# Optimization experiments

Measured on AMD Instinct MI355X. Metric: run time of the kernel, lower is better.

## Reference

```python
import jax, jax.numpy as jnp
import numpy as np

N_CONTENT = 100000
N_USER = 100000
N_EDGES = 1600000
D_CONTENT = 256
D_USER = 128
HIDDEN = 128
OUT = 64


def setup_inputs() -> dict:
    key = jax.random.key(0)
    ks = jax.random.split(key, 12)
    s = lambda d: 1.0 / np.sqrt(d)
    return {
        "x_content": jax.random.normal(ks[0], (N_CONTENT, D_CONTENT), jnp.float32),
        "x_user": jax.random.normal(ks[1], (N_USER, D_USER), jnp.float32),
        # edge_index[0] = source (user) ids, edge_index[1] = destination (content) ids
        "edge_index": jax.random.randint(ks[2], (2, N_EDGES), 0, N_CONTENT, jnp.int64),
        # per-node-type input projections
        "Wc": jax.random.normal(ks[3], (D_CONTENT, HIDDEN), jnp.float32) * s(D_CONTENT),
        "bc": jnp.zeros((HIDDEN,), jnp.float32),
        "Wu": jax.random.normal(ks[4], (D_USER, HIDDEN), jnp.float32) * s(D_USER),
        "bu": jnp.zeros((HIDDEN,), jnp.float32),
        # SAGEConv: W_l applied to aggregated neighbor features (with bias),
        # W_r applied to root/self features (no bias, per PyG default)
        "Wl": jax.random.normal(ks[5], (HIDDEN, HIDDEN), jnp.float32) * s(HIDDEN),
        "bl": jnp.zeros((HIDDEN,), jnp.float32),
        "Wr": jax.random.normal(ks[6], (HIDDEN, HIDDEN), jnp.float32) * s(HIDDEN),
        # final output projection on content nodes
        "Wo": jax.random.normal(ks[7], (HIDDEN, OUT), jnp.float32) * s(HIDDEN),
        "bo": jnp.zeros((OUT,), jnp.float32),
    }


def reference(x_content, x_user, edge_index, Wc, bc, Wu, bu, Wl, bl, Wr, Wo, bo):
    # Per-node-type linear + relu
    h_c = jax.nn.relu(x_content @ Wc + bc)  # [Nc, H]
    h_u = jax.nn.relu(x_user @ Wu + bu)      # [Nu, H]

    src, dst = edge_index[0], edge_index[1]
    # SAGEConv mean aggregation: gather user features along edges, scatter-mean to content
    msg = h_u[src]                                              # [E, H] gather
    agg = jax.ops.segment_sum(msg, dst, num_segments=N_CONTENT) # [Nc, H]
    cnt = jax.ops.segment_sum(jnp.ones((msg.shape[0],), msg.dtype), dst,
                              num_segments=N_CONTENT)
    mean = agg / jnp.maximum(cnt, 1.0)[:, None]                 # 0 for isolated nodes

    h = mean @ Wl + bl + h_c @ Wr                               # SAGE combine
    return h @ Wo + bo                                          # [Nc, OUT]
```

## Files before the change

kernel.cpp:

```cpp
#include <hip/hip_runtime.h>
#include <hip/hip_bf16.h>

#define NC 100000
#define NU 100000
#define NE 1600000
#define DC 256
#define DU 128
#define HID 128
#define OUTD 64

#define BSHIFT 9
#define BRANGE 512
#define NBUCK ((NC + BRANGE - 1) / BRANGE)
#define BCAP 10240
#define EPB 8192
#define ABLK ((NE + EPB - 1) / EPB)

#define TM 32
#define NT_C (NC / TM)
#define NT_U (NU / TM)

#define SH (HID + 8)

typedef __attribute__((ext_vector_type(8))) short bf16x8;
typedef __attribute__((ext_vector_type(4))) float f32x4;

__device__ inline unsigned short f2b(float f) {
    unsigned int u = __float_as_uint(f);
    u += 0x7fffu + ((u >> 16) & 1u);
    return (unsigned short)(u >> 16);
}

__global__ void prep_kernel(const float* __restrict__ Wl, const float* __restrict__ bl,
                            const float* __restrict__ Wr, const float* __restrict__ Wo,
                            const float* __restrict__ bo,
                            __hip_bfloat16* __restrict__ Wlo_p,
                            __hip_bfloat16* __restrict__ Wro_p,
                            float* __restrict__ b2) {
    const int k = blockIdx.x;
    const int t = threadIdx.x;
    const int f = t & 63, j4 = t >> 6;
    __shared__ float red[3][4][OUTD];
    float a0 = 0.f, a1 = 0.f, s = 0.f;
    for (int m = j4 * 32; m < j4 * 32 + 32; ++m) {
        float wo = Wo[m * OUTD + f];
        a0 = fmaf(Wl[k * HID + m], wo, a0);
        a1 = fmaf(Wr[k * HID + m], wo, a1);
        s = fmaf(bl[m], wo, s);
    }
    red[0][j4][f] = a0; red[1][j4][f] = a1; red[2][j4][f] = s;
    __syncthreads();
    if (j4 == 0) {
        a0 = red[0][0][f] + red[0][1][f] + red[0][2][f] + red[0][3][f];
        a1 = red[1][0][f] + red[1][1][f] + red[1][2][f] + red[1][3][f];
        const int wv = f >> 4, l16 = f & 15;
        const int ks = k >> 5, quad = (k >> 3) & 3, e = k & 7;
        const int idx = (((wv * 4 + ks) * 64) + quad * 16 + l16) * 8 + e;
        Wlo_p[idx] = __float2bfloat16(a0);
        Wro_p[idx] = __float2bfloat16(a1);
        if (k == 0)
            b2[f] = bo[f] + red[2][0][f] + red[2][1][f] + red[2][2][f] + red[2][3][f];
    }
}

__global__ void pack_w(const float* __restrict__ W, __hip_bfloat16* __restrict__ Wp,
                       int K) {
    int i = blockIdx.x * blockDim.x + threadIdx.x;
    int total = K * HID;
    if (i >= total) return;
    int j = i % HID, k = i / HID;
    int nks = K >> 5;
    int idx = (((j >> 4) * nks + (k >> 5)) * 64 + ((k >> 3) & 3) * 16 + (j & 15)) * 8 +
              (k & 7);
    Wp[idx] = __float2bfloat16(W[k * HID + j]);
}

template <int DIN, bool BF16OUT>
__device__ __forceinline__ void gemm_path(const float* __restrict__ x,
                                          const __hip_bfloat16* __restrict__ W1p,
                                          const float* __restrict__ b1,
                                          const __hip_bfloat16* __restrict__ W2p,
                                          const float* __restrict__ bias2,
                                          void* __restrict__ outp, int tile,
                                          short* __restrict__ smem) {
    constexpr int NKS = DIN / 32;
    constexpr int SA = DIN + 8;
    constexpr int CPR = DIN / 8;
    constexpr int RSTEP = 256 / CPR;
    constexpr int NCH = TM / RSTEP;
    short* a_s = smem;
    short* h_s = smem + TM * SA;

    const int t = threadIdx.x;
    const int w = t >> 6, lane = t & 63;
    const int quad = lane >> 4, l16 = lane & 15;
    const int r0 = t / CPR, c0 = t % CPR;
    const int base = tile * TM;

    bf16x8 b1f[2][NKS];
#pragma unroll
    for (int ntl = 0; ntl < 2; ++ntl)
#pragma unroll
        for (int ks = 0; ks < NKS; ++ks)
            b1f[ntl][ks] =
                *(const bf16x8*)&W1p[(size_t)(((2 * w + ntl) * NKS + ks) * 64 + lane) * 8];
    bf16x8 b2f[HID / 32];
#pragma unroll
    for (int ks = 0; ks < HID / 32; ++ks)
        b2f[ks] = *(const bf16x8*)&W2p[(size_t)((w * 4 + ks) * 64 + lane) * 8];
    const float bb1_0 = b1[w * 32 + l16];
    const float bb1_1 = b1[w * 32 + 16 + l16];
    const float bb2 = BF16OUT ? 0.f : bias2[w * 16 + l16];

    float4 va[NCH][2];
#pragma unroll
    for (int k = 0; k < NCH; ++k) {
        const float4* p = (const float4*)(x + (size_t)(base + r0 + k * RSTEP) * DIN + c0 * 8);
        va[k][0] = p[0];
        va[k][1] = p[1];
    }
#pragma unroll
    for (int k = 0; k < NCH; ++k) {
        bf16x8 a;
        a[0] = (short)f2b(va[k][0].x); a[1] = (short)f2b(va[k][0].y);
        a[2] = (short)f2b(va[k][0].z); a[3] = (short)f2b(va[k][0].w);
        a[4] = (short)f2b(va[k][1].x); a[5] = (short)f2b(va[k][1].y);
        a[6] = (short)f2b(va[k][1].z); a[7] = (short)f2b(va[k][1].w);
        *(bf16x8*)&a_s[(r0 + k * RSTEP) * SA + c0 * 8] = a;
    }
    __syncthreads();

#pragma unroll
    for (int rg = 0; rg < TM / 16; ++rg) {
        bf16x8 af[NKS];
#pragma unroll
        for (int ks = 0; ks < NKS; ++ks)
            af[ks] = *(const bf16x8*)&a_s[(rg * 16 + l16) * SA + ks * 32 + quad * 8];
        f32x4 acc0 = (f32x4){0.f, 0.f, 0.f, 0.f};
        f32x4 acc1 = (f32x4){0.f, 0.f, 0.f, 0.f};
#pragma unroll
        for (int ks = 0; ks < NKS; ++ks) {
            acc0 = __builtin_amdgcn_mfma_f32_16x16x32_bf16(af[ks], b1f[0][ks], acc0, 0, 0, 0);
            acc1 = __builtin_amdgcn_mfma_f32_16x16x32_bf16(af[ks], b1f[1][ks], acc1, 0, 0, 0);
        }
#pragma unroll
        for (int r = 0; r < 4; ++r) {
            int row = rg * 16 + quad * 4 + r;
            h_s[row * SH + w * 32 + l16] = (short)f2b(fmaxf(acc0[r] + bb1_0, 0.f));
            h_s[row * SH + w * 32 + 16 + l16] = (short)f2b(fmaxf(acc1[r] + bb1_1, 0.f));
        }
    }
    __syncthreads();

#pragma unroll
    for (int rg = 0; rg < TM / 16; ++rg) {
        f32x4 acc = (f32x4){0.f, 0.f, 0.f, 0.f};
#pragma unroll
        for (int ks = 0; ks < HID / 32; ++ks) {
            bf16x8 a = *(const bf16x8*)&h_s[(rg * 16 + l16) * SH + ks * 32 + quad * 8];
            acc = __builtin_amdgcn_mfma_f32_16x16x32_bf16(a, b2f[ks], acc, 0, 0, 0);
        }
#pragma unroll
        for (int r = 0; r < 4; ++r) {
            int rr = base + rg * 16 + quad * 4 + r;
            if (BF16OUT)
                ((unsigned short*)outp)[(size_t)rr * OUTD + w * 16 + l16] = f2b(acc[r]);
            else
                ((float*)outp)[(size_t)rr * OUTD + w * 16 + l16] = acc[r] + bb2;
        }
    }
}

__global__ void __launch_bounds__(256, 4) dual_gemm(
    const float* __restrict__ xc, const __hip_bfloat16* __restrict__ Wc_p,
    const float* __restrict__ bc, const __hip_bfloat16* __restrict__ Wro_p,
    const float* __restrict__ b2, float* __restrict__ out,
    const float* __restrict__ xu, const __hip_bfloat16* __restrict__ Wu_p,
    const float* __restrict__ bu, const __hip_bfloat16* __restrict__ Wlo_p,
    unsigned short* __restrict__ pu) {
    __shared__ __align__(16) short smem[TM * (DC + 8) + TM * (HID + 8)];
    int b = blockIdx.x;
    if (b < NT_C)
        gemm_path<DC, false>(xc, Wc_p, bc, Wro_p, b2, out, b, smem);
    else
        gemm_path<DU, true>(xu, Wu_p, bu, Wlo_p, nullptr, pu, b - NT_C, smem);
}

__global__ void __launch_bounds__(256) bucket_a(const int* __restrict__ src,
                                                const int* __restrict__ dst,
                                                int* __restrict__ gcur,
                                                unsigned int* __restrict__ bke) {
    __shared__ unsigned int pk[EPB];
    __shared__ int hist[NBUCK];
    __shared__ int lbase[NBUCK];
    __shared__ int lcur[NBUCK];
    __shared__ int gb[NBUCK];
    __shared__ int ts[256];
    const int t = threadIdx.x;
    const int base = blockIdx.x * EPB;
    for (int i = t; i < NBUCK; i += 256) hist[i] = 0;
    __syncthreads();
#pragma unroll
    for (int k = 0; k < EPB / 256; ++k) {
        int e = base + k * 256 + t;
        if (e < NE) atomicAdd(&hist[dst[e] >> BSHIFT], 1);
    }
    __syncthreads();
    int h = (t < NBUCK) ? hist[t] : 0;
    ts[t] = h;
    __syncthreads();
    for (int d = 1; d < 256; d <<= 1) {
        int x = (t >= d) ? ts[t - d] : 0;
        __syncthreads();
        ts[t] += x;
        __syncthreads();
    }
    if (t < NBUCK) {
        int ex = ts[t] - h;
        lbase[t] = ex;
        lcur[t] = ex;
        gb[t] = atomicAdd(&gcur[t], h);
    }
    __syncthreads();
#pragma unroll
    for (int k = 0; k < EPB / 256; ++k) {
        int e = base + k * 256 + t;
        if (e < NE) {
            int s = src[e], d = dst[e];
            int b = d >> BSHIFT;
            int p = atomicAdd(&lcur[b], 1);
            pk[p] = ((unsigned int)s << BSHIFT) | (unsigned int)(d & (BRANGE - 1));
        }
    }
    __syncthreads();
    const int wv = t >> 6, ln = t & 63;
    for (int b = wv; b < NBUCK; b += 4) {
        int s0 = lbase[b], c = hist[b], g0 = gb[b];
        for (int j = ln; j < c; j += 64) {
            int pos = g0 + j;
            if (pos < BCAP) bke[(size_t)b * BCAP + pos] = pk[s0 + j];
        }
    }
}

__global__ void scan_mid(const int* __restrict__ gcur, int* __restrict__ gbase,
                         int* __restrict__ off) {
    __shared__ int ts[256];
    int t = threadIdx.x;
    int h = (t < NBUCK) ? gcur[t] : 0;
    ts[t] = h;
    __syncthreads();
    for (int d = 1; d < 256; d <<= 1) {
        int x = (t >= d) ? ts[t - d] : 0;
        __syncthreads();
        ts[t] += x;
        __syncthreads();
    }
    if (t < NBUCK) gbase[t] = ts[t] - h;
    if (t == 0) { gbase[NBUCK] = NE; off[NC] = NE; }
}

__global__ void __launch_bounds__(256) bucket_b(const int* __restrict__ gcur,
                                                const int* __restrict__ gbase,
                                                const unsigned int* __restrict__ bke,
                                                int* __restrict__ off,
                                                int* __restrict__ ssrc) {
    __shared__ unsigned int pk[BCAP];
    __shared__ int hist[BRANGE];
    __shared__ int hb[BRANGE];
    __shared__ int cur[BRANGE];
    __shared__ int ts[256];
    const int t = threadIdx.x;
    const int b = blockIdx.x;
    const int n = min(gcur[b], BCAP);
    const int g0 = gbase[b];
    for (int i = t; i < n; i += 256) pk[i] = bke[(size_t)b * BCAP + i];
    for (int i = t; i < BRANGE; i += 256) hist[i] = 0;
    __syncthreads();
    for (int i = t; i < n; i += 256) atomicAdd(&hist[pk[i] & (BRANGE - 1)], 1);
    __syncthreads();
    int a0 = hist[2 * t], a1 = hist[2 * t + 1];
    int s = a0 + a1;
    ts[t] = s;
    __syncthreads();
    for (int d = 1; d < 256; d <<= 1) {
        int x = (t >= d) ? ts[t - d] : 0;
        __syncthreads();
        ts[t] += x;
        __syncthreads();
    }
    int ex = ts[t] - s;
    hb[2 * t] = ex;
    hb[2 * t + 1] = ex + a0;
    __syncthreads();
    for (int i = t; i < BRANGE; i += 256) {
        int node = b * BRANGE + i;
        cur[i] = g0 + hb[i];
        if (node < NC) off[node] = g0 + hb[i];
    }
    __syncthreads();
    for (int i = t; i < n; i += 256) {
        unsigned int v = pk[i];
        int p = atomicAdd(&cur[v & (BRANGE - 1)], 1);
        ssrc[p] = (int)(v >> BSHIFT);
    }
}

__global__ void __launch_bounds__(256) gather_agg(const int* __restrict__ ssrc,
                                                  const int* __restrict__ off,
                                                  const unsigned int* __restrict__ pu,
                                                  float* __restrict__ out) {
    int node = blockIdx.x * 4 + (threadIdx.x >> 6);
    if (node >= NC) return;
    int lane = threadIdx.x & 63;
    int g = lane >> 3;
    int f8 = lane & 7;
    int e0 = off[node], e1 = off[node + 1];
    float acc[8] = {0.f, 0.f, 0.f, 0.f, 0.f, 0.f, 0.f, 0.f};
    for (int e = e0 + g; e < e1; e += 8) {
        int s = ssrc[e];
        uint4 v = ((const uint4*)pu)[(size_t)s * 8 + f8];
        acc[0] += __uint_as_float(v.x << 16);
        acc[1] += __uint_as_float(v.x & 0xffff0000u);
        acc[2] += __uint_as_float(v.y << 16);
        acc[3] += __uint_as_float(v.y & 0xffff0000u);
        acc[4] += __uint_as_float(v.z << 16);
        acc[5] += __uint_as_float(v.z & 0xffff0000u);
        acc[6] += __uint_as_float(v.w << 16);
        acc[7] += __uint_as_float(v.w & 0xffff0000u);
    }
#pragma unroll
    for (int m = 8; m <= 32; m <<= 1) {
#pragma unroll
        for (int j = 0; j < 8; ++j) acc[j] += __shfl_xor(acc[j], m, 64);
    }
    if (g == 0) {
        float inv = 1.0f / (float)max(e1 - e0, 1);
        float4* po = (float4*)(out + (size_t)node * OUTD + f8 * 8);
        float4 o0 = po[0], o1 = po[1];
        o0.x += acc[0] * inv; o0.y += acc[1] * inv;
        o0.z += acc[2] * inv; o0.w += acc[3] * inv;
        o1.x += acc[4] * inv; o1.y += acc[5] * inv;
        o1.z += acc[6] * inv; o1.w += acc[7] * inv;
        po[0] = o0; po[1] = o1;
    }
}

extern "C" void kernel_launch(void* const* d_in, const int* in_sizes, int n_in,
                              void* d_out, int out_size, void* d_ws, size_t ws_size,
                              hipStream_t stream) {
    const float* xc = (const float*)d_in[0];
    const float* xu = (const float*)d_in[1];
    const int*   ei = (const int*)d_in[2];
    const float* Wc = (const float*)d_in[3];
    const float* bc = (const float*)d_in[4];
    const float* Wu = (const float*)d_in[5];
    const float* bu = (const float*)d_in[6];
    const float* Wl = (const float*)d_in[7];
    const float* bl = (const float*)d_in[8];
    const float* Wr = (const float*)d_in[9];
    const float* Wo = (const float*)d_in[10];
    const float* bo = (const float*)d_in[11];
    float* out = (float*)d_out;

    const int* esrc = ei;
    const int* edst = ei + NE;

    unsigned short* pu = (unsigned short*)d_ws;
    int* ssrc  = (int*)(pu + (size_t)NU * OUTD);
    unsigned int* bke = (unsigned int*)(ssrc + NE);
    int* gcur  = (int*)(bke + (size_t)NBUCK * BCAP);
    int* gbase = gcur + NBUCK;
    int* off   = gcur + 400;
    float* b2  = (float*)(off + NC + 4);
    __hip_bfloat16* Wlo_p = (__hip_bfloat16*)(b2 + OUTD);
    __hip_bfloat16* Wro_p = Wlo_p + OUTD * HID;
    __hip_bfloat16* Wu_p  = Wro_p + OUTD * HID;
    __hip_bfloat16* Wc_p  = Wu_p + HID * DU;

    hipMemsetAsync(gcur, 0, NBUCK * sizeof(int), stream);

    prep_kernel<<<HID, 256, 0, stream>>>(Wl, bl, Wr, Wo, bo, Wlo_p, Wro_p, b2);
    pack_w<<<(DU * HID + 255) / 256, 256, 0, stream>>>(Wu, Wu_p, DU);
    pack_w<<<(DC * HID + 255) / 256, 256, 0, stream>>>(Wc, Wc_p, DC);

    dual_gemm<<<NT_C + NT_U, 256, 0, stream>>>(xc, Wc_p, bc, Wro_p, b2, out,
                                               xu, Wu_p, bu, Wlo_p, pu);

    bucket_a<<<ABLK, 256, 0, stream>>>(esrc, edst, gcur, bke);
    scan_mid<<<1, 256, 0, stream>>>(gcur, gbase, off);
    bucket_b<<<NBUCK, 256, 0, stream>>>(gcur, gbase, bke, off, ssrc);
    gather_agg<<<(NC + 3) / 4, 256, 0, stream>>>(ssrc, off, (const unsigned int*)pu, out);
}
```

Before: 334.1 us.

## Replace two-pass bucket sort with global counting sort fused into GEMM launch

```diff
diff --git a/kernel.cpp b/kernel.cpp
--- a/kernel.cpp
+++ b/kernel.cpp
@@ -9,18 +9,14 @@
 #define HID 128
 #define OUTD 64
 
-#define BSHIFT 9
-#define BRANGE 512
-#define NBUCK ((NC + BRANGE - 1) / BRANGE)
-#define BCAP 10240
-#define EPB 8192
-#define ABLK ((NE + EPB - 1) / EPB)
-
 #define TM 32
 #define NT_C (NC / TM)
 #define NT_U (NU / TM)
+#define NHB 256
 
 #define SH (HID + 8)
+
+#define SCAN_TILE 16384
 
 typedef __attribute__((ext_vector_type(8))) short bf16x8;
 typedef __attribute__((ext_vector_type(4))) float f32x4;
@@ -171,138 +167,93 @@
     }
 }
 
-__global__ void __launch_bounds__(256, 4) dual_gemm(
+__global__ void __launch_bounds__(256, 4) fused_gemm_hist(
     const float* __restrict__ xc, const __hip_bfloat16* __restrict__ Wc_p,
     const float* __restrict__ bc, const __hip_bfloat16* __restrict__ Wro_p,
     const float* __restrict__ b2, float* __restrict__ out,
     const float* __restrict__ xu, const __hip_bfloat16* __restrict__ Wu_p,
     const float* __restrict__ bu, const __hip_bfloat16* __restrict__ Wlo_p,
-    unsigned short* __restrict__ pu) {
+    unsigned short* __restrict__ pu,
+    const int* __restrict__ edst, int* __restrict__ cnt) {
     __shared__ __align__(16) short smem[TM * (DC + 8) + TM * (HID + 8)];
     int b = blockIdx.x;
+    if (b < NHB) {
+        int i = b * 256 + threadIdx.x;
+        for (; i < NE; i += NHB * 256) atomicAdd(&cnt[edst[i]], 1);
+        return;
+    }
+    b -= NHB;
     if (b < NT_C)
         gemm_path<DC, false>(xc, Wc_p, bc, Wro_p, b2, out, b, smem);
     else
         gemm_path<DU, true>(xu, Wu_p, bu, Wlo_p, nullptr, pu, b - NT_C, smem);
 }
 
-__global__ void __launch_bounds__(256) bucket_a(const int* __restrict__ src,
-                                                const int* __restrict__ dst,
-                                                int* __restrict__ gcur,
-                                                unsigned int* __restrict__ bke) {
-    __shared__ unsigned int pk[EPB];
-    __shared__ int hist[NBUCK];
-    __shared__ int lbase[NBUCK];
-    __shared__ int lcur[NBUCK];
-    __shared__ int gb[NBUCK];
-    __shared__ int ts[256];
+__global__ void __launch_bounds__(1024) scan_off(const int* __restrict__ cnt,
+                                                 int* __restrict__ off,
+                                                 int* __restrict__ cur) {
+    __shared__ int tile[SCAN_TILE];
+    __shared__ int wsum[16];
+    __shared__ int wbase[16];
+    __shared__ int carry;
     const int t = threadIdx.x;
-    const int base = blockIdx.x * EPB;
-    for (int i = t; i < NBUCK; i += 256) hist[i] = 0;
+    const int lane = t & 63, wv = t >> 6;
+    if (t == 0) carry = 0;
     __syncthreads();
-#pragma unroll
-    for (int k = 0; k < EPB / 256; ++k) {
-        int e = base + k * 256 + t;
-        if (e < NE) atomicAdd(&hist[dst[e] >> BSHIFT], 1);
-    }
-    __syncthreads();
-    int h = (t < NBUCK) ? hist[t] : 0;
-    ts[t] = h;
-    __syncthreads();
-    for (int d = 1; d < 256; d <<= 1) {
-        int x = (t >= d) ? ts[t - d] : 0;
-        __syncthreads();
-        ts[t] += x;
-        __syncthreads();
-    }
-    if (t < NBUCK) {
-        int ex = ts[t] - h;
-        lbase[t] = ex;
-        lcur[t] = ex;
-        gb[t] = atomicAdd(&gcur[t], h);
-    }
-    __syncthreads();
-#pragma unroll
-    for (int k = 0; k < EPB / 256; ++k) {
-        int e = base + k * 256 + t;
-        if (e < NE) {
-            int s = src[e], d = dst[e];
-            int b = d >> BSHIFT;
-            int p = atomicAdd(&lcur[b], 1);
-            pk[p] = ((unsigned int)s << BSHIFT) | (unsigned int)(d & (BRANGE - 1));
-        }
-    }
-    __syncthreads();
-    const int wv = t >> 6, ln = t & 63;
-    for (int b = wv; b < NBUCK; b += 4) {
-        int s0 = lbase[b], c = hist[b], g0 = gb[b];
-        for (int j = ln; j < c; j += 64) {
-            int pos = g0 + j;
-            if (pos < BCAP) bke[(size_t)b * BCAP + pos] = pk[s0 + j];
-        }
-    }
-}
-
-__global__ void scan_mid(const int* __restrict__ gcur, int* __restrict__ gbase,
-                         int* __restrict__ off) {
-    __shared__ int ts[256];
-    int t = threadIdx.x;
-    int h = (t < NBUCK) ? gcur[t] : 0;
-    ts[t] = h;
-    __syncthreads();
-    for (int d = 1; d < 256; d <<= 1) {
-        int x = (t >= d) ? ts[t - d] : 0;
-        __syncthreads();
-        ts[t] += x;
-        __syncthreads();
-    }
-    if (t < NBUCK) gbase[t] = ts[t] - h;
-    if (t == 0) { gbase[NBUCK] = NE; off[NC] = NE; }
-}
-
-__global__ void __launch_bounds__(256) bucket_b(const int* __restrict__ gcur,
-                                                const int* __restrict__ gbase,
-                                                const unsigned int* __restrict__ bke,
-                                                int* __restrict__ off,
-                                                int* __restrict__ ssrc) {
-    __shared__ unsigned int pk[BCAP];
-    __shared__ int hist[BRANGE];
-    __shared__ int hb[BRANGE];
-    __shared__ int cur[BRANGE];
-    __shared__ int ts[256];
-    const int t = threadIdx.x;
-    const int b = blockIdx.x;
-    const int n = min(gcur[b], BCAP);
-    const int g0 = gbase[b];
-    for (int i = t; i < n; i += 256) pk[i] = bke[(size_t)b * BCAP + i];
-    for (int i = t; i < BRANGE; i += 256) hist[i] = 0;
-    __syncthreads();
-    for (int i = t; i < n; i += 256) atomicAdd(&hist[pk[i] & (BRANGE - 1)], 1);
-    __syncthreads();
-    int a0 = hist[2 * t], a1 = hist[2 * t + 1];
-    int s = a0 + a1;
-    ts[t] = s;
-    __syncthreads();
-    for (int d = 1; d < 256; d <<= 1) {
-        int x = (t >= d) ? ts[t - d] : 0;
-        __syncthreads();
-        ts[t] += x;
-        __syncthreads();
-    }
-    int ex = ts[t] - s;
-    hb[2 * t] = ex;
-    hb[2 * t + 1] = ex + a0;
-    __syncthreads();
-    for (int i = t; i < BRANGE; i += 256) {
-        int node = b * BRANGE + i;
-        cur[i] = g0 + hb[i];
-        if (node < NC) off[node] = g0 + hb[i];
-    }
-    __syncthreads();
-    for (int i = t; i < n; i += 256) {
-        unsigned int v = pk[i];
-        int p = atomicAdd(&cur[v & (BRANGE - 1)], 1);
-        ssrc[p] = (int)(v >> BSHIFT);
+    for (int t0 = 0; t0 < NC; t0 += SCAN_TILE) {
+        const int n = min(SCAN_TILE, NC - t0);
+        for (int i = t; i < n; i += 1024) tile[i] = cnt[t0 + i];
+        __syncthreads();
+        const int b0 = t * 16;
+        int s = 0;
+        if (b0 < n) {
+            int m = min(16, n - b0);
+#pragma unroll
+            for (int j = 0; j < 16; ++j)
+                if (j < m) { int v = tile[b0 + j]; tile[b0 + j] = s; s += v; }
+        }
+        int inc = s;
+#pragma unroll
+        for (int d = 1; d < 64; d <<= 1) {
+            int x = __shfl_up(inc, d, 64);
+            if (lane >= d) inc += x;
+        }
+        if (lane == 63) wsum[wv] = inc;
+        __syncthreads();
+        if (t == 0) {
+            int r = 0;
+            for (int i = 0; i < 16; ++i) { int v = wsum[i]; wbase[i] = r; r += v; }
+            wsum[0] = r;
+        }
+        __syncthreads();
+        const int base = carry + wbase[wv] + (inc - s);
+        if (b0 < n) {
+            int m = min(16, n - b0);
+#pragma unroll
+            for (int j = 0; j < 16; ++j)
+                if (j < m) {
+                    int v = base + tile[b0 + j];
+                    off[t0 + b0 + j] = v;
+                    cur[t0 + b0 + j] = v;
+                }
+        }
+        __syncthreads();
+        if (t == 0) carry += wsum[0];
+        __syncthreads();
+    }
+    if (t == 0) off[NC] = NE;
+}
+
+__global__ void __launch_bounds__(256) scatter_edges(const int* __restrict__ src,
+                                                     const int* __restrict__ dst,
+                                                     int* __restrict__ cur,
+                                                     int* __restrict__ ssrc) {
+    int i = blockIdx.x * 256 + threadIdx.x;
+    const int stride = gridDim.x * 256;
+    for (; i < NE; i += stride) {
+        int d = dst[i];
+        int p = atomicAdd(&cur[d], 1);
+        ssrc[p] = src[i];
     }
 }
 
@@ -316,10 +267,34 @@
     int g = lane >> 3;
     int f8 = lane & 7;
     int e0 = off[node], e1 = off[node + 1];
+    const uint4* pu4 = (const uint4*)pu;
     float acc[8] = {0.f, 0.f, 0.f, 0.f, 0.f, 0.f, 0.f, 0.f};
-    for (int e = e0 + g; e < e1; e += 8) {
+    int e = e0 + g;
+    for (; e + 8 < e1; e += 16) {
+        int s0 = ssrc[e];
+        int s1 = ssrc[e + 8];
+        uint4 v0 = pu4[(size_t)s0 * 8 + f8];
+        uint4 v1 = pu4[(size_t)s1 * 8 + f8];
+        acc[0] += __uint_as_float(v0.x << 16);
+        acc[1] += __uint_as_float(v0.x & 0xffff0000u);
+        acc[2] += __uint_as_float(v0.y << 16);
+        acc[3] += __uint_as_float(v0.y & 0xffff0000u);
+        acc[4] += __uint_as_float(v0.z << 16);
+        acc[5] += __uint_as_float(v0.z & 0xffff0000u);
+        acc[6] += __uint_as_float(v0.w << 16);
+        acc[7] += __uint_as_float(v0.w & 0xffff0000u);
+        acc[0] += __uint_as_float(v1.x << 16);
+        acc[1] += __uint_as_float(v1.x & 0xffff0000u);
+        acc[2] += __uint_as_float(v1.y << 16);
+        acc[3] += __uint_as_float(v1.y & 0xffff0000u);
+        acc[4] += __uint_as_float(v1.z << 16);
+        acc[5] += __uint_as_float(v1.z & 0xffff0000u);
+        acc[6] += __uint_as_float(v1.w << 16);
+        acc[7] += __uint_as_float(v1.w & 0xffff0000u);
+    }
+    if (e < e1) {
         int s = ssrc[e];
-        uint4 v = ((const uint4*)pu)[(size_t)s * 8 + f8];
+        uint4 v = pu4[(size_t)s * 8 + f8];
         acc[0] += __uint_as_float(v.x << 16);
         acc[1] += __uint_as_float(v.x & 0xffff0000u);
         acc[2] += __uint_as_float(v.y << 16);
@@ -367,28 +342,26 @@
     const int* edst = ei + NE;
 
     unsigned short* pu = (unsigned short*)d_ws;
-    int* ssrc  = (int*)(pu + (size_t)NU * OUTD);
-    unsigned int* bke = (unsigned int*)(ssrc + NE);
-    int* gcur  = (int*)(bke + (size_t)NBUCK * BCAP);
-    int* gbase = gcur + NBUCK;
-    int* off   = gcur + 400;
-    float* b2  = (float*)(off + NC + 4);
+    int* ssrc = (int*)(pu + (size_t)NU * OUTD);
+    int* cnt  = ssrc + NE;
+    int* cur  = cnt + NC;
+    int* off  = cur + NC;
+    float* b2 = (float*)(off + NC + 4);
     __hip_bfloat16* Wlo_p = (__hip_bfloat16*)(b2 + OUTD);
     __hip_bfloat16* Wro_p = Wlo_p + OUTD * HID;
     __hip_bfloat16* Wu_p  = Wro_p + OUTD * HID;
     __hip_bfloat16* Wc_p  = Wu_p + HID * DU;
 
-    hipMemsetAsync(gcur, 0, NBUCK * sizeof(int), stream);
+    hipMemsetAsync(cnt, 0, NC * sizeof(int), stream);
 
     prep_kernel<<<HID, 256, 0, stream>>>(Wl, bl, Wr, Wo, bo, Wlo_p, Wro_p, b2);
     pack_w<<<(DU * HID + 255) / 256, 256, 0, stream>>>(Wu, Wu_p, DU);
     pack_w<<<(DC * HID + 255) / 256, 256, 0, stream>>>(Wc, Wc_p, DC);
 
-    dual_gemm<<<NT_C + NT_U, 256, 0, stream>>>(xc, Wc_p, bc, Wro_p, b2, out,
-                                               xu, Wu_p, bu, Wlo_p, pu);
-
-    bucket_a<<<ABLK, 256, 0, stream>>>(esrc, edst, gcur, bke);
-    scan_mid<<<1, 256, 0, stream>>>(gcur, gbase, off);
-    bucket_b<<<NBUCK, 256, 0, stream>>>(gcur, gbase, bke, off, ssrc);
+    fused_gemm_hist<<<NHB + NT_C + NT_U, 256, 0, stream>>>(
+        xc, Wc_p, bc, Wro_p, b2, out, xu, Wu_p, bu, Wlo_p, pu, edst, cnt);
+
+    scan_off<<<1, 1024, 0, stream>>>(cnt, off, cur);
+    scatter_edges<<<2048, 256, 0, stream>>>(esrc, edst, cur, ssrc);
     gather_agg<<<(NC + 3) / 4, 256, 0, stream>>>(ssrc, off, (const unsigned int*)pu, out);
 }
```

Result: slower. 480.1 us (+43.7%).

## Fuse edge bucketing into GEMM launch and merge bucket sort with gather

Applied to the files above, without the earlier changes.

```diff
diff --git a/kernel.cpp b/kernel.cpp
--- a/kernel.cpp
+++ b/kernel.cpp
@@ -9,18 +9,20 @@
 #define HID 128
 #define OUTD 64
 
-#define BSHIFT 9
-#define BRANGE 512
+#define BSHIFT 7
+#define BRANGE 128
 #define NBUCK ((NC + BRANGE - 1) / BRANGE)
-#define BCAP 10240
-#define EPB 8192
-#define ABLK ((NE + EPB - 1) / EPB)
+#define BCAP 4096
+#define EPB 4096
+#define NBA ((NE + EPB - 1) / EPB)
 
 #define TM 32
 #define NT_C (NC / TM)
 #define NT_U (NU / TM)
 
 #define SH (HID + 8)
+
+#define SMEM_FUSED 29920
 
 typedef __attribute__((ext_vector_type(8))) short bf16x8;
 typedef __attribute__((ext_vector_type(4))) float f32x4;
@@ -31,48 +33,59 @@
     return (unsigned short)(u >> 16);
 }
 
-__global__ void prep_kernel(const float* __restrict__ Wl, const float* __restrict__ bl,
-                            const float* __restrict__ Wr, const float* __restrict__ Wo,
-                            const float* __restrict__ bo,
-                            __hip_bfloat16* __restrict__ Wlo_p,
-                            __hip_bfloat16* __restrict__ Wro_p,
-                            float* __restrict__ b2) {
-    const int k = blockIdx.x;
+__global__ void __launch_bounds__(256) prep_all(
+    const float* __restrict__ Wl, const float* __restrict__ bl,
+    const float* __restrict__ Wr, const float* __restrict__ Wo,
+    const float* __restrict__ bo, const float* __restrict__ Wu,
+    const float* __restrict__ Wc, __hip_bfloat16* __restrict__ Wlo_p,
+    __hip_bfloat16* __restrict__ Wro_p, float* __restrict__ b2,
+    __hip_bfloat16* __restrict__ Wu_p, __hip_bfloat16* __restrict__ Wc_p,
+    int* __restrict__ gcur) {
+    __shared__ float red[3][4][OUTD];
+    const int b = blockIdx.x;
     const int t = threadIdx.x;
-    const int f = t & 63, j4 = t >> 6;
-    __shared__ float red[3][4][OUTD];
-    float a0 = 0.f, a1 = 0.f, s = 0.f;
-    for (int m = j4 * 32; m < j4 * 32 + 32; ++m) {
-        float wo = Wo[m * OUTD + f];
-        a0 = fmaf(Wl[k * HID + m], wo, a0);
-        a1 = fmaf(Wr[k * HID + m], wo, a1);
-        s = fmaf(bl[m], wo, s);
-    }
-    red[0][j4][f] = a0; red[1][j4][f] = a1; red[2][j4][f] = s;
-    __syncthreads();
-    if (j4 == 0) {
-        a0 = red[0][0][f] + red[0][1][f] + red[0][2][f] + red[0][3][f];
-        a1 = red[1][0][f] + red[1][1][f] + red[1][2][f] + red[1][3][f];
-        const int wv = f >> 4, l16 = f & 15;
-        const int ks = k >> 5, quad = (k >> 3) & 3, e = k & 7;
-        const int idx = (((wv * 4 + ks) * 64) + quad * 16 + l16) * 8 + e;
-        Wlo_p[idx] = __float2bfloat16(a0);
-        Wro_p[idx] = __float2bfloat16(a1);
-        if (k == 0)
-            b2[f] = bo[f] + red[2][0][f] + red[2][1][f] + red[2][2][f] + red[2][3][f];
-    }
-}
-
-__global__ void pack_w(const float* __restrict__ W, __hip_bfloat16* __restrict__ Wp,
-                       int K) {
-    int i = blockIdx.x * blockDim.x + threadIdx.x;
-    int total = K * HID;
-    if (i >= total) return;
-    int j = i % HID, k = i / HID;
-    int nks = K >> 5;
-    int idx = (((j >> 4) * nks + (k >> 5)) * 64 + ((k >> 3) & 3) * 16 + (j & 15)) * 8 +
-              (k & 7);
-    Wp[idx] = __float2bfloat16(W[k * HID + j]);
+    if (b < HID) {
+        const int k = b;
+        const int f = t & 63, j4 = t >> 6;
+        float a0 = 0.f, a1 = 0.f, s = 0.f;
+        for (int m = j4 * 32; m < j4 * 32 + 32; ++m) {
+            float wo = Wo[m * OUTD + f];
+            a0 = fmaf(Wl[k * HID + m], wo, a0);
+            a1 = fmaf(Wr[k * HID + m], wo, a1);
+            s = fmaf(bl[m], wo, s);
+        }
+        red[0][j4][f] = a0; red[1][j4][f] = a1; red[2][j4][f] = s;
+        __syncthreads();
+        if (j4 == 0) {
+            a0 = red[0][0][f] + red[0][1][f] + red[0][2][f] + red[0][3][f];
+            a1 = red[1][0][f] + red[1][1][f] + red[1][2][f] + red[1][3][f];
+            const int wv = f >> 4, l16 = f & 15;
+            const int ks = k >> 5, quad = (k >> 3) & 3, e = k & 7;
+            const int idx = (((wv * 4 + ks) * 64) + quad * 16 + l16) * 8 + e;
+            Wlo_p[idx] = __float2bfloat16(a0);
+            Wro_p[idx] = __float2bfloat16(a1);
+            if (k == 0)
+                b2[f] = bo[f] + red[2][0][f] + red[2][1][f] + red[2][2][f] + red[2][3][f];
+        }
+        return;
+    }
+    if (b == HID)
+        for (int j = t; j < NBUCK; j += 256) gcur[j] = 0;
+    int i = (b - HID) * 256 + t;
+    if (i < DU * HID) {
+        int j = i % HID, k = i / HID;
+        int idx = (((j >> 4) * (DU / 32) + (k >> 5)) * 64 + ((k >> 3) & 3) * 16 +
+                   (j & 15)) * 8 + (k & 7);
+        Wu_p[idx] = __float2bfloat16(Wu[k * HID + j]);
+    } else {
+        int i2 = i - DU * HID;
+        if (i2 < DC * HID) {
+            int j = i2 % HID, k = i2 / HID;
+            int idx = (((j >> 4) * (DC / 32) + (k >> 5)) * 64 + ((k >> 3) & 3) * 16 +
+                       (j & 15)) * 8 + (k & 7);
+            Wc_p[idx] = __float2bfloat16(Wc[k * HID + j]);
+        }
+    }
 }
 
 template <int DIN, bool BF16OUT>
@@ -171,42 +184,116 @@
     }
 }
 
-__global__ void __launch_bounds__(256, 4) dual_gemm(
+__device__ void bucket_a_path(const int* __restrict__ src, const int* __restrict__ dst,
+                              int* __restrict__ gcur, unsigned int* __restrict__ bke,
+                              int blk, char* __restrict__ sm) {
+    unsigned int* pk = (unsigned int*)sm;
+    int* hist  = (int*)(sm + EPB * 4);
+    int* lbase = hist + NBUCK;
+    int* lcur  = lbase + NBUCK;
+    int* gb    = lcur + NBUCK;
+    int* ts    = gb + NBUCK;
+    const int t = threadIdx.x;
+    const int base = blk * EPB;
+
+    for (int i = t; i < NBUCK; i += 256) hist[i] = 0;
+    __syncthreads();
+#pragma unroll
+    for (int k = 0; k < EPB / 256; ++k) {
+        int e = base + k * 256 + t;
+        if (e < NE) atomicAdd(&hist[dst[e] >> BSHIFT], 1);
+    }
+    __syncthreads();
+    int h[4];
+    int s = 0;
+#pragma unroll
+    for (int j = 0; j < 4; ++j) {
+        int idx = 4 * t + j;
+        h[j] = (idx < NBUCK) ? hist[idx] : 0;
+        s += h[j];
+    }
+    ts[t] = s;
+    __syncthreads();
+    for (int d = 1; d < 256; d <<= 1) {
+        int x = (t >= d) ? ts[t - d] : 0;
+        __syncthreads();
+        ts[t] += x;
+        __syncthreads();
+    }
+    int ex = ts[t] - s;
+#pragma unroll
+    for (int j = 0; j < 4; ++j) {
+        int idx = 4 * t + j;
+        if (idx < NBUCK) {
+            lbase[idx] = ex;
+            lcur[idx] = ex;
+            if (h[j] > 0) gb[idx] = atomicAdd(&gcur[idx], h[j]);
+            ex += h[j];
+        }
+    }
+    __syncthreads();
+#pragma unroll
+    for (int k = 0; k < EPB / 256; ++k) {
+        int e = base + k * 256 + t;
+        if (e < NE) {
+            int sv = src[e], d = dst[e];
+            int bb = d >> BSHIFT;
+            int p = atomicAdd(&lcur[bb], 1);
+            pk[p] = ((unsigned int)sv << BSHIFT) | (unsigned int)(d & (BRANGE - 1));
+        }
+    }
+    __syncthreads();
+    const int wv = t >> 6, ln = t & 63;
+    for (int bb = wv; bb < NBUCK; bb += 4) {
+        int s0 = lbase[bb], c = hist[bb], g0 = gb[bb];
+        for (int j = ln; j < c; j += 64) {
+            int pos = g0 + j;
+            if (pos < BCAP) bke[(size_t)bb * BCAP + pos] = pk[s0 + j];
+        }
+    }
+}
+
+__global__ void __launch_bounds__(256, 4) fused_main(
     const float* __restrict__ xc, const __hip_bfloat16* __restrict__ Wc_p,
     const float* __restrict__ bc, const __hip_bfloat16* __restrict__ Wro_p,
     const float* __restrict__ b2, float* __restrict__ out,
     const float* __restrict__ xu, const __hip_bfloat16* __restrict__ Wu_p,
     const float* __restrict__ bu, const __hip_bfloat16* __restrict__ Wlo_p,
-    unsigned short* __restrict__ pu) {
-    __shared__ __align__(16) short smem[TM * (DC + 8) + TM * (HID + 8)];
+    unsigned short* __restrict__ pu,
+    const int* __restrict__ esrc, const int* __restrict__ edst,
+    int* __restrict__ gcur, unsigned int* __restrict__ bke) {
+    __shared__ __align__(16) char smem[SMEM_FUSED];
     int b = blockIdx.x;
+    if (b < NBA) {
+        bucket_a_path(esrc, edst, gcur, bke, b, smem);
+        return;
+    }
+    b -= NBA;
     if (b < NT_C)
-        gemm_path<DC, false>(xc, Wc_p, bc, Wro_p, b2, out, b, smem);
+        gemm_path<DC, false>(xc, Wc_p, bc, Wro_p, b2, out, b, (short*)smem);
     else
-        gemm_path<DU, true>(xu, Wu_p, bu, Wlo_p, nullptr, pu, b - NT_C, smem);
-}
-
-__global__ void __launch_bounds__(256) bucket_a(const int* __restrict__ src,
-                                                const int* __restrict__ dst,
-                                                int* __restrict__ gcur,
-                                                unsigned int* __restrict__ bke) {
-    __shared__ unsigned int pk[EPB];
-    __shared__ int hist[NBUCK];
-    __shared__ int lbase[NBUCK];
-    __shared__ int lcur[NBUCK];
-    __shared__ int gb[NBUCK];
+        gemm_path<DU, true>(xu, Wu_p, bu, Wlo_p, nullptr, pu, b - NT_C, (short*)smem);
+}
+
+__global__ void __launch_bounds__(256) bucket_gather(
+    const int* __restrict__ gcur, const unsigned int* __restrict__ bke,
+    const unsigned int* __restrict__ pu, float* __restrict__ out) {
+    __shared__ unsigned int pk[BCAP];
+    __shared__ int sl[BCAP];
+    __shared__ int hist[BRANGE];
+    __shared__ int hb[BRANGE + 1];
+    __shared__ int cur[BRANGE];
     __shared__ int ts[256];
     const int t = threadIdx.x;
-    const int base = blockIdx.x * EPB;
-    for (int i = t; i < NBUCK; i += 256) hist[i] = 0;
-    __syncthreads();
-#pragma unroll
-    for (int k = 0; k < EPB / 256; ++k) {
-        int e = base + k * 256 + t;
-        if (e < NE) atomicAdd(&hist[dst[e] >> BSHIFT], 1);
-    }
-    __syncthreads();
-    int h = (t < NBUCK) ? hist[t] : 0;
+    const int b = blockIdx.x;
+    const int n = min(gcur[b], BCAP);
+
+    for (int i = t; i < n; i += 256) pk[i] = bke[(size_t)b * BCAP + i];
+    if (t < BRANGE) hist[t] = 0;
+    __syncthreads();
+    for (int i = t; i < n; i += 256) atomicAdd(&hist[pk[i] & (BRANGE - 1)], 1);
+    __syncthreads();
+    int h = (t < BRANGE) ? hist[t] : 0;
     ts[t] = h;
     __syncthreads();
     for (int d = 1; d < 256; d <<= 1) {
@@ -215,134 +302,77 @@
         ts[t] += x;
         __syncthreads();
     }
-    if (t < NBUCK) {
-        int ex = ts[t] - h;
-        lbase[t] = ex;
-        lcur[t] = ex;
-        gb[t] = atomicAdd(&gcur[t], h);
-    }
-    __syncthreads();
-#pragma unroll
-    for (int k = 0; k < EPB / 256; ++k) {
-        int e = base + k * 256 + t;
-        if (e < NE) {
-            int s = src[e], d = dst[e];
-            int b = d >> BSHIFT;
-            int p = atomicAdd(&lcur[b], 1);
-            pk[p] = ((unsigned int)s << BSHIFT) | (unsigned int)(d & (BRANGE - 1));
-        }
-    }
-    __syncthreads();
-    const int wv = t >> 6, ln = t & 63;
-    for (int b = wv; b < NBUCK; b += 4) {
-        int s0 = lbase[b], c = hist[b], g0 = gb[b];
-        for (int j = ln; j < c; j += 64) {
-            int pos = g0 + j;
-            if (pos < BCAP) bke[(size_t)b * BCAP + pos] = pk[s0 + j];
-        }
-    }
-}
-
-__global__ void scan_mid(const int* __restrict__ gcur, int* __restrict__ gbase,
-                         int* __restrict__ off) {
-    __shared__ int ts[256];
-    int t = threadIdx.x;
-    int h = (t < NBUCK) ? gcur[t] : 0;
-    ts[t] = h;
-    __syncthreads();
-    for (int d = 1; d < 256; d <<= 1) {
-        int x = (t >= d) ? ts[t - d] : 0;
-        __syncthreads();
-        ts[t] += x;
-        __syncthreads();
-    }
-    if (t < NBUCK) gbase[t] = ts[t] - h;
-    if (t == 0) { gbase[NBUCK] = NE; off[NC] = NE; }
-}
-
-__global__ void __launch_bounds__(256) bucket_b(const int* __restrict__ gcur,
-                                                const int* __restrict__ gbase,
-                                                const unsigned int* __restrict__ bke,
-                                                int* __restrict__ off,
-                                                int* __restrict__ ssrc) {
-    __shared__ unsigned int pk[BCAP];
-    __shared__ int hist[BRANGE];
-    __shared__ int hb[BRANGE];
-    __shared__ int cur[BRANGE];
-    __shared__ int ts[256];
-    const int t = threadIdx.x;
-    const int b = blockIdx.x;
-    const int n = min(gcur[b], BCAP);
-    const int g0 = gbase[b];
-    for (int i = t; i < n; i += 256) pk[i] = bke[(size_t)b * BCAP + i];
-    for (int i = t; i < BRANGE; i += 256) hist[i] = 0;
-    __syncthreads();
-    for (int i = t; i < n; i += 256) atomicAdd(&hist[pk[i] & (BRANGE - 1)], 1);
-    __syncthreads();
-    int a0 = hist[2 * t], a1 = hist[2 * t + 1];
-    int s = a0 + a1;
-    ts[t] = s;
-    __syncthreads();
-    for (int d = 1; d < 256; d <<= 1) {
-        int x = (t >= d) ? ts[t - d] : 0;
-        __syncthreads();
-        ts[t] += x;
-        __syncthreads();
-    }
-    int ex = ts[t] - s;
-    hb[2 * t] = ex;
-    hb[2 * t + 1] = ex + a0;
-    __syncthreads();
-    for (int i = t; i < BRANGE; i += 256) {
-        int node = b * BRANGE + i;
-        cur[i] = g0 + hb[i];
-        if (node < NC) off[node] = g0 + hb[i];
-    }
+    if (t < BRANGE) {
+        hb[t] = ts[t] - h;
+        cur[t] = ts[t] - h;
+    }
+    if (t == 0) hb[BRANGE] = n;
     __syncthreads();
     for (int i = t; i < n; i += 256) {
         unsigned int v = pk[i];
         int p = atomicAdd(&cur[v & (BRANGE - 1)], 1);
-        ssrc[p] = (int)(v >> BSHIFT);
-    }
-}
-
-__global__ void __launch_bounds__(256) gather_agg(const int* __restrict__ ssrc,
-                                                  const int* __restrict__ off,
-                                                  const unsigned int* __restrict__ pu,
-                                                  float* __restrict__ out) {
-    int node = blockIdx.x * 4 + (threadIdx.x >> 6);
-    if (node >= NC) return;
-    int lane = threadIdx.x & 63;
-    int g = lane >> 3;
-    int f8 = lane & 7;
-    int e0 = off[node], e1 = off[node + 1];
-    float acc[8] = {0.f, 0.f, 0.f, 0.f, 0.f, 0.f, 0.f, 0.f};
-    for (int e = e0 + g; e < e1; e += 8) {
-        int s = ssrc[e];
-        uint4 v = ((const uint4*)pu)[(size_t)s * 8 + f8];
-        acc[0] += __uint_as_float(v.x << 16);
-        acc[1] += __uint_as_float(v.x & 0xffff0000u);
-        acc[2] += __uint_as_float(v.y << 16);
-        acc[3] += __uint_as_float(v.y & 0xffff0000u);
-        acc[4] += __uint_as_float(v.z << 16);
-        acc[5] += __uint_as_float(v.z & 0xffff0000u);
-        acc[6] += __uint_as_float(v.w << 16);
-        acc[7] += __uint_as_float(v.w & 0xffff0000u);
-    }
-#pragma unroll
-    for (int m = 8; m <= 32; m <<= 1) {
-#pragma unroll
-        for (int j = 0; j < 8; ++j) acc[j] += __shfl_xor(acc[j], m, 64);
-    }
-    if (g == 0) {
-        float inv = 1.0f / (float)max(e1 - e0, 1);
-        float4* po = (float4*)(out + (size_t)node * OUTD + f8 * 8);
-        float4 o0 = po[0], o1 = po[1];
-        o0.x += acc[0] * inv; o0.y += acc[1] * inv;
-        o0.z += acc[2] * inv; o0.w += acc[3] * inv;
-        o1.x += acc[4] * inv; o1.y += acc[5] * inv;
-        o1.z += acc[6] * inv; o1.w += acc[7] * inv;
-        po[0] = o0; po[1] = o1;
+        sl[p] = (int)(v >> BSHIFT);
+    }
+    __syncthreads();
+
+    const int wv = t >> 6, lane = t & 63;
+    const int g = lane >> 3, f8 = lane & 7;
+    const int node0 = b * BRANGE;
+    const int nn = min(BRANGE, NC - node0);
+    const uint4* pu4 = (const uint4*)pu;
+    for (int i = wv; i < nn; i += 4) {
+        const int e0 = hb[i], e1 = hb[i + 1];
+        float acc[8] = {0.f, 0.f, 0.f, 0.f, 0.f, 0.f, 0.f, 0.f};
+        int e = e0 + g;
+        for (; e + 8 < e1; e += 16) {
+            int s0 = sl[e];
+            int s1 = sl[e + 8];
+            uint4 v0 = pu4[(size_t)s0 * 8 + f8];
+            uint4 v1 = pu4[(size_t)s1 * 8 + f8];
+            acc[0] += __uint_as_float(v0.x << 16);
+            acc[1] += __uint_as_float(v0.x & 0xffff0000u);
+            acc[2] += __uint_as_float(v0.y << 16);
+            acc[3] += __uint_as_float(v0.y & 0xffff0000u);
+            acc[4] += __uint_as_float(v0.z << 16);
+            acc[5] += __uint_as_float(v0.z & 0xffff0000u);
+            acc[6] += __uint_as_float(v0.w << 16);
+            acc[7] += __uint_as_float(v0.w & 0xffff0000u);
+            acc[0] += __uint_as_float(v1.x << 16);
+            acc[1] += __uint_as_float(v1.x & 0xffff0000u);
+            acc[2] += __uint_as_float(v1.y << 16);
+            acc[3] += __uint_as_float(v1.y & 0xffff0000u);
+            acc[4] += __uint_as_float(v1.z << 16);
+            acc[5] += __uint_as_float(v1.z & 0xffff0000u);
+            acc[6] += __uint_as_float(v1.w << 16);
+            acc[7] += __uint_as_float(v1.w & 0xffff0000u);
+        }
+        if (e < e1) {
+            int s = sl[e];
+            uint4 v = pu4[(size_t)s * 8 + f8];
+            acc[0] += __uint_as_float(v.x << 16);
+            acc[1] += __uint_as_float(v.x & 0xffff0000u);
+            acc[2] += __uint_as_float(v.y << 16);
+            acc[3] += __uint_as_float(v.y & 0xffff0000u);
+            acc[4] += __uint_as_float(v.z << 16);
+            acc[5] += __uint_as_float(v.z & 0xffff0000u);
+            acc[6] += __uint_as_float(v.w << 16);
+            acc[7] += __uint_as_float(v.w & 0xffff0000u);
+        }
+#pragma unroll
+        for (int m = 8; m <= 32; m <<= 1) {
+#pragma unroll
+            for (int j = 0; j < 8; ++j) acc[j] += __shfl_xor(acc[j], m, 64);
+        }
+        if (g == 0) {
+            float inv = 1.0f / (float)max(e1 - e0, 1);
+            float4* po = (float4*)(out + (size_t)(node0 + i) * OUTD + f8 * 8);
+            float4 o0 = po[0], o1 = po[1];
+            o0.x += acc[0] * inv; o0.y += acc[1] * inv;
+            o0.z += acc[2] * inv; o0.w += acc[3] * inv;
+            o1.x += acc[4] * inv; o1.y += acc[5] * inv;
+            o1.z += acc[6] * inv; o1.w += acc[7] * inv;
+            po[0] = o0; po[1] = o1;
+        }
     }
 }
 
@@ -367,28 +397,19 @@
     const int* edst = ei + NE;
 
     unsigned short* pu = (unsigned short*)d_ws;
-    int* ssrc  = (int*)(pu + (size_t)NU * OUTD);
-    unsigned int* bke = (unsigned int*)(ssrc + NE);
-    int* gcur  = (int*)(bke + (size_t)NBUCK * BCAP);
-    int* gbase = gcur + NBUCK;
-    int* off   = gcur + 400;
-    float* b2  = (float*)(off + NC + 4);
+    unsigned int* bke = (unsigned int*)(pu + (size_t)NU * OUTD);
+    int* gcur = (int*)(bke + (size_t)NBUCK * BCAP);
+    float* b2 = (float*)(gcur + 784);
     __hip_bfloat16* Wlo_p = (__hip_bfloat16*)(b2 + OUTD);
     __hip_bfloat16* Wro_p = Wlo_p + OUTD * HID;
     __hip_bfloat16* Wu_p  = Wro_p + OUTD * HID;
     __hip_bfloat16* Wc_p  = Wu_p + HID * DU;
 
-    hipMemsetAsync(gcur, 0, NBUCK * sizeof(int), stream);
-
-    prep_kernel<<<HID, 256, 0, stream>>>(Wl, bl, Wr, Wo, bo, Wlo_p, Wro_p, b2);
-    pack_w<<<(DU * HID + 255) / 256, 256, 0, stream>>>(Wu, Wu_p, DU);
-    pack_w<<<(DC * HID + 255) / 256, 256, 0, stream>>>(Wc, Wc_p, DC);
-
-    dual_gemm<<<NT_C + NT_U, 256, 0, stream>>>(xc, Wc_p, bc, Wro_p, b2, out,
-                                               xu, Wu_p, bu, Wlo_p, pu);
-
-    bucket_a<<<ABLK, 256, 0, stream>>>(esrc, edst, gcur, bke);
-    scan_mid<<<1, 256, 0, stream>>>(gcur, gbase, off);
-    bucket_b<<<NBUCK, 256, 0, stream>>>(gcur, gbase, bke, off, ssrc);
-    gather_agg<<<(NC + 3) / 4, 256, 0, stream>>>(ssrc, off, (const unsigned int*)pu, out);
-}
+    prep_all<<<HID + (DU * HID + DC * HID) / 256, 256, 0, stream>>>(
+        Wl, bl, Wr, Wo, bo, Wu, Wc, Wlo_p, Wro_p, b2, Wu_p, Wc_p, gcur);
+
+    fused_main<<<NBA + NT_C + NT_U, 256, 0, stream>>>(
+        xc, Wc_p, bc, Wro_p, b2, out, xu, Wu_p, bu, Wlo_p, pu, esrc, edst, gcur, bke);
+
+    bucket_gather<<<NBUCK, 256, 0, stream>>>(gcur, bke, (const unsigned int*)pu, out);
+}
```

New measurement: 365.9 us. 1.1x slower.
